# Kernel optimization log

Measured on AMD Instinct MI355X. Metric: run time of the kernel, lower is better.

## Reference

```python
import jax, jax.numpy as jnp
import numpy as np

B, F0, D = 1024, 32, 32
HID = [128, 128, 128]


def setup_inputs() -> dict:
    key = jax.random.key(0)
    ks = jax.random.split(key, 4)
    inputs = jax.random.normal(ks[0], (B, F0, D), dtype=jnp.float32)
    # glorot-like init for conv filters, flattened to (F0*Fk, H)
    def glorot(k, fan_in, fan_out):
        lim = np.sqrt(6.0 / (fan_in + fan_out)).astype(np.float32)
        return jax.random.uniform(k, (fan_in, fan_out), dtype=jnp.float32, minval=-lim, maxval=lim)
    W0 = glorot(ks[1], F0 * F0, HID[0])
    W1 = glorot(ks[2], F0 * HID[0], HID[1])
    W2 = glorot(ks[3], F0 * HID[1], HID[2])
    b0 = jnp.zeros((HID[0],), dtype=jnp.float32)
    b1 = jnp.zeros((HID[1],), dtype=jnp.float32)
    b2 = jnp.zeros((HID[2],), dtype=jnp.float32)
    return {"inputs": inputs, "W0": W0, "W1": W1, "W2": W2,
            "b0": b0, "b1": b1, "b2": b2,
            "field_size": F0, "embedding_size": D}


def _cin_layer(x0, state, W, b):
    # x0: (B, F0, D), state: (B, Fk, D)
    bsz, f0, d = x0.shape
    fk = state.shape[1]
    # per-embedding-dim outer product; flatten (f0, fk) row-major to match
    # tf reshape of matmul(state_split_0, state_split_k^T)
    z = jnp.einsum('bfd,bgd->bdfg', x0, state).reshape(bsz, d, f0 * fk)
    h = z @ W + b  # (B, D, H); 1x1 conv1d == matmul over f0*fk
    # activation is linear (identity)
    return jnp.transpose(h, (0, 2, 1))  # (B, H, D)


def reference(inputs, W0, W1, W2, b0, b1, b2, field_size, embedding_size):
    x0 = inputs.reshape(-1, field_size, embedding_size)
    state = x0
    outputs = []
    for W, b in ((W0, b0), (W1, b1), (W2, b2)):
        fm = _cin_layer(x0, state, W, b)
        state = fm          # skip=False: state and output are the full map
        outputs.append(fm)
    # concat over field axis, sum over embedding dim -> (B, sum(H))
    return jnp.sum(jnp.concatenate(outputs, axis=1), axis=-1)
```

## Files before the change

### kernel.cpp

```cpp
#include <hip/hip_runtime.h>
#include <hip/hip_bf16.h>


typedef __attribute__((ext_vector_type(8))) short short8;
typedef __attribute__((ext_vector_type(8))) __bf16 bf16x8;
typedef __attribute__((ext_vector_type(16))) float f32x16;
typedef __attribute__((ext_vector_type(4))) unsigned short u16x4;

#define DEVINL static __device__ __forceinline__

DEVINL unsigned short f2bf_rne(float f) {
  unsigned int u = __builtin_bit_cast(unsigned int, f);
  unsigned int r = u + 0x7fffu + ((u >> 16) & 1u);
  return (unsigned short)(r >> 16);
}

template <typename V>
DEVINL auto mfma_32x32x16_bf16(V a, V b, f32x16 c, int)
    -> decltype(__builtin_amdgcn_mfma_f32_32x32x16_bf16(a, b, c, 0, 0, 0)) {
  return __builtin_amdgcn_mfma_f32_32x32x16_bf16(a, b, c, 0, 0, 0);
}
template <typename V>
DEVINL f32x16 mfma_32x32x16_bf16(V a, V b, f32x16 c, long) {
  return __builtin_amdgcn_mfma_f32_32x32x16_bf16(
      __builtin_bit_cast(bf16x8, a), __builtin_bit_cast(bf16x8, b), c, 0, 0, 0);
}
DEVINL f32x16 mfma_bf16(short8 a, short8 b, f32x16 c) {
  return mfma_32x32x16_bf16(a, b, c, 0);
}

__global__ void pack_w_kernel(const float* __restrict__ W0,
                              const float* __restrict__ W1,
                              const float* __restrict__ W2,
                              unsigned short* __restrict__ Wt) {
  __shared__ float tile[8][132];
  const int u = blockIdx.x;
  const float* W; int FK, f, kb, base;
  if (u < 128)      { W = W0; FK = 32;  f = u >> 2;         kb = u & 3;          base = 0; }
  else if (u < 640) { W = W1; FK = 128; f = (u - 128) >> 4; kb = (u - 128) & 15; base = 131072; }
  else              { W = W2; FK = 128; f = (u - 640) >> 4; kb = (u - 640) & 15; base = 655360; }
  const int t = threadIdx.x;
#pragma unroll
  for (int i = 0; i < 4; ++i) {
    const int e = t + i * 256;
    const int kk = e >> 7, h = e & 127;
    tile[kk][h] = W[(f * FK + kb * 8 + kk) * 128 + h];
  }
  __syncthreads();
  unsigned short* dst = Wt + base + f * (FK / 8) * 1024 + kb * 1024;
  const int h = t >> 1;
  const int j0 = (t & 1) * 4;
  u16x4 v;
  v.x = f2bf_rne(tile[j0 + 0][h]);
  v.y = f2bf_rne(tile[j0 + 1][h]);
  v.z = f2bf_rne(tile[j0 + 2][h]);
  v.w = f2bf_rne(tile[j0 + 3][h]);
  *(u16x4*)&dst[t * 4] = v;
}

template <int KQ, int LAYER>
DEVINL void run_layer(const unsigned short* __restrict__ WtL,
                      const float* __restrict__ bias,
                      const float* __restrict__ x0g,
                      float* __restrict__ outp, int outoff,
                      unsigned int* SB,
                      int wgb0, int mrow, int bw, int l31, int half) {
  __syncthreads();

  int4 sfr[KQ];
  const int r = bw * 32 + l31;
#pragma unroll
  for (int kq = 0; kq < KQ; ++kq) {
    const int row0 = kq * 8 + half * 4;
    int4 v;
    v.x = (int)SB[(row0 + 0) * 128 + r];
    v.y = (int)SB[(row0 + 1) * 128 + r];
    v.z = (int)SB[(row0 + 2) * 128 + r];
    v.w = (int)SB[(row0 + 3) * 128 + r];
    sfr[kq] = v;
  }

  f32x16 zv;
#pragma unroll
  for (int e = 0; e < 16; ++e) zv[e] = 0.f;
  f32x16 outacc = zv;

  const char* gb = (const char*)WtL +
                   (size_t)(half * 2048 + (mrow * 32 + l31) * 16);
  const int xb = (wgb0 + bw) * 1024 + l31;

  auto ldq = [&](short8* wv, int q) {
#pragma unroll
    for (int i = 0; i < 4; ++i)
      wv[i] = *(const short8*)(gb + (size_t)q * 16384 + i * 4096);
  };

  short8 wa[4], wb[4];

  if constexpr (KQ == 8) {
    float xs = x0g[xb];
    ldq(wa, 0);
    ldq(wb, 1);
    __syncthreads();

#pragma unroll 1
    for (int f = 0; f < 32; ++f) {
      float xn = xs;
      if (f < 31) xn = x0g[xb + (f + 1) * 32];
      f32x16 Y;
#pragma unroll
      for (int i = 0; i < 4; ++i) {
        const short8 s = __builtin_bit_cast(short8, sfr[i]);
        Y = mfma_bf16(wa[i], s, i == 0 ? zv : Y);
      }
      if (f < 31) ldq(wa, 2 * f + 2);
#pragma unroll
      for (int i = 0; i < 4; ++i) {
        const short8 s = __builtin_bit_cast(short8, sfr[4 + i]);
        Y = mfma_bf16(wb[i], s, Y);
      }
      if (f < 31) ldq(wb, 2 * f + 3);
#pragma unroll
      for (int e = 0; e < 16; ++e) outacc[e] += xs * Y[e];
      xs = xn;
    }
  } else {
    float xa0 = x0g[xb], xa1 = x0g[xb + 32];
    ldq(wa, 0);
    __syncthreads();

    const short8 s0 = __builtin_bit_cast(short8, sfr[0]);
    const short8 s1 = __builtin_bit_cast(short8, sfr[KQ - 1]);
    auto doQ = [&](const short8* wv, float xA, float xB) {
      f32x16 Y = mfma_bf16(wv[0], s0, zv);
      Y = mfma_bf16(wv[1], s1, Y);
#pragma unroll
      for (int e = 0; e < 16; ++e) outacc[e] += xA * Y[e];
      Y = mfma_bf16(wv[2], s0, zv);
      Y = mfma_bf16(wv[3], s1, Y);
#pragma unroll
      for (int e = 0; e < 16; ++e) outacc[e] += xB * Y[e];
    };

#pragma unroll 1
    for (int q2 = 0; q2 < 8; ++q2) {
      const int q = 2 * q2;
      const float xm0 = x0g[xb + (2 * q + 2) * 32];
      const float xm1 = x0g[xb + (2 * q + 3) * 32];
      ldq(wb, q + 1);
      float xn0 = xa0, xn1 = xa1;
      if (q2 < 7) {
        xn0 = x0g[xb + (2 * q + 4) * 32];
        xn1 = x0g[xb + (2 * q + 5) * 32];
      }
      doQ(wa, xa0, xa1);
      if (q2 < 7) ldq(wa, q + 2);
      doQ(wb, xm0, xm1);
      xa0 = xn0; xa1 = xn1;
    }
  }

  float bv[16];
#pragma unroll
  for (int e = 0; e < 16; ++e)
    bv[e] = bias[mrow * 32 + (e & 3) + 8 * (e >> 2) + 4 * half];

  if constexpr (LAYER < 2) {
#pragma unroll
    for (int g = 0; g < 4; ++g) {
      const int h2 = mrow * 16 + 4 * g + 2 * half;
      const float v0 = outacc[4 * g + 0] + bv[4 * g + 0];
      const float v1 = outacc[4 * g + 1] + bv[4 * g + 1];
      const float v2 = outacc[4 * g + 2] + bv[4 * g + 2];
      const float v3 = outacc[4 * g + 3] + bv[4 * g + 3];
      SB[h2 * 128 + r] = (unsigned)f2bf_rne(v0) | ((unsigned)f2bf_rne(v1) << 16);
      SB[(h2 + 1) * 128 + r] =
          (unsigned)f2bf_rne(v2) | ((unsigned)f2bf_rne(v3) << 16);
    }
  }

  float sv[16];
#pragma unroll
  for (int e = 0; e < 16; ++e) {
    float v = outacc[e];
    v += __shfl_xor(v, 1);
    v += __shfl_xor(v, 2);
    v += __shfl_xor(v, 4);
    v += __shfl_xor(v, 8);
    v += __shfl_xor(v, 16);
    sv[e] = v + 32.0f * bv[e];
  }
  if (l31 == 0) {
#pragma unroll
    for (int g = 0; g < 4; ++g) {
      const int h = mrow * 32 + 8 * g + 4 * half;
      float4 o = {sv[4 * g + 0], sv[4 * g + 1], sv[4 * g + 2], sv[4 * g + 3]};
      *(float4*)&outp[bw * 384 + outoff + h] = o;
    }
  }
}

DEVINL void run_layer2_fast(const unsigned short* __restrict__ WtL,
                            const float* __restrict__ bias,
                            const float* __restrict__ x0g,
                            float* __restrict__ outp,
                            unsigned int* SB, int wgb0,
                            int w, int l31, int half, int tid) {
  __syncthreads();

  f32x16 zv;
#pragma unroll
  for (int e = 0; e < 16; ++e) zv[e] = 0.f;

  const int bw = w >> 2, gt = w & 3;
  short8 a1[2];
  {
    const float* xr = &x0g[(size_t)(wgb0 + bw) * 1024 + l31 * 32];
#pragma unroll
    for (int kq = 0; kq < 2; ++kq) {
      const int d0 = kq * 16 + half * 8;
      union { short8 v; unsigned short u[8]; } t;
#pragma unroll
      for (int j = 0; j < 8; ++j) t.u[j] = f2bf_rne(xr[d0 + j]);
      a1[kq] = t.v;
    }
  }
  short8 bfr[2];
  {
    const int g = gt * 32 + l31;
    const unsigned int* row = &SB[(g >> 1) * 128 + bw * 32];
    const int sh = (g & 1) * 16;
#pragma unroll
    for (int kq = 0; kq < 2; ++kq) {
      const int d0 = kq * 16 + half * 8;
      union { short8 v; unsigned short u[8]; } t;
#pragma unroll
      for (int j = 0; j < 8; ++j)
        t.u[j] = (unsigned short)(row[d0 + j] >> sh);
      bfr[kq] = t.v;
    }
  }
  f32x16 ua = mfma_bf16(a1[0], bfr[0], zv);
  ua = mfma_bf16(a1[1], bfr[1], ua);
  __syncthreads();

  unsigned short* U16 = (unsigned short*)SB;
  {
    const int g = gt * 32 + l31;
#pragma unroll
    for (int reg = 0; reg < 16; ++reg) {
      const int f = (reg & 3) + 8 * (reg >> 2) + 4 * half;
      const int k = f * 128 + g;
      U16[(k >> 1) * 8 + bw * 2 + (k & 1)] = f2bf_rne(ua[reg]);
    }
  }
  __syncthreads();

  const int mt = w & 3, kh = w >> 2;
  const char* gb = (const char*)WtL +
                   (size_t)(half * 2048 + (mt * 32 + l31) * 16);
  const int bl = l31 & 3;

  auto ldq2 = [&](short8* wv, int q) {
#pragma unroll
    for (int i = 0; i < 4; ++i)
      wv[i] = *(const short8*)(gb + (size_t)q * 16384 + i * 4096);
  };
  auto breadq = [&](short8* bv, int q) {
#pragma unroll
    for (int i = 0; i < 4; ++i) {
      const int row0 = (q * 4 + i) * 8 + half * 4;
      int4 v;
      v.x = (int)SB[(row0 + 0) * 4 + bl];
      v.y = (int)SB[(row0 + 1) * 4 + bl];
      v.z = (int)SB[(row0 + 2) * 4 + bl];
      v.w = (int)SB[(row0 + 3) * 4 + bl];
      bv[i] = __builtin_bit_cast(short8, v);
    }
  };

  f32x16 acc0 = zv, acc1 = zv;
  short8 qa[4], qb[4], Ba[4], Bb[4];
  const int q0 = kh * 16;
  ldq2(qa, q0);
  breadq(Ba, q0);
#pragma unroll 1
  for (int qq = 0; qq < 8; ++qq) {
    const int q = q0 + 2 * qq;
    ldq2(qb, q + 1);
    breadq(Bb, q + 1);
#pragma unroll
    for (int i = 0; i < 4; ++i) acc0 = mfma_bf16(qa[i], Ba[i], acc0);
    if (qq < 7) {
      ldq2(qa, q + 2);
      breadq(Ba, q + 2);
    }
#pragma unroll
    for (int i = 0; i < 4; ++i) acc1 = mfma_bf16(qb[i], Bb[i], acc1);
  }
#pragma unroll
  for (int e = 0; e < 16; ++e) acc0[e] += acc1[e];

  __syncthreads();

  float* P = (float*)SB;
  if (l31 < 4) {
#pragma unroll
    for (int reg = 0; reg < 16; ++reg) {
      const int h = mt * 32 + (reg & 3) + 8 * (reg >> 2) + 4 * half;
      P[(l31 * 128 + h) * 4 + kh] = acc0[reg];
    }
  }
  __syncthreads();
  if (tid < 512) {
    const int b = tid >> 7, h = tid & 127;
    const float v = P[tid * 4] + P[tid * 4 + 1] + P[tid * 4 + 2] +
                    P[tid * 4 + 3] + 32.0f * bias[h];
    outp[b * 384 + 256 + h] = v;
  }
}

__global__ __launch_bounds__(1024, 1) void cin_kernel(
    const float* __restrict__ x0g, const unsigned short* __restrict__ Wt,
    const float* __restrict__ b0, const float* __restrict__ b1,
    const float* __restrict__ b2, float* __restrict__ out) {
  __shared__ unsigned int SB[64 * 128];

  const int t = threadIdx.x;
  const int lane = t & 63;
  const int w = t >> 6;
  const int mrow = w & 3;
  const int bw = w >> 2;
  const int l31 = lane & 31, half = lane >> 5;
  const int wgb0 = blockIdx.x * 4;

#pragma unroll
  for (int s = 0; s < 2; ++s) {
    const int i = t + s * 1024;
    const int r = i & 127, g2 = i >> 7;
    const float* p = &x0g[(wgb0 + (r >> 5)) * 1024 + (2 * g2) * 32 + (r & 31)];
    SB[g2 * 128 + r] =
        (unsigned)f2bf_rne(p[0]) | ((unsigned)f2bf_rne(p[32]) << 16);
  }

  float* outp = out + (size_t)wgb0 * 384;
  run_layer<2, 0>(Wt, b0, x0g, outp, 0, SB, wgb0, mrow, bw, l31, half);
  run_layer<8, 1>(Wt + 131072, b1, x0g, outp, 128, SB,
                  wgb0, mrow, bw, l31, half);
  run_layer2_fast(Wt + 655360, b2, x0g, outp, SB, wgb0, w, l31, half, t);
}

extern "C" void kernel_launch(void* const* d_in, const int* in_sizes, int n_in,
                              void* d_out, int out_size, void* d_ws, size_t ws_size,
                              hipStream_t stream) {
  (void)in_sizes; (void)n_in; (void)out_size; (void)ws_size;
  const float* x0 = (const float*)d_in[0];
  const float* W0 = (const float*)d_in[1];
  const float* W1 = (const float*)d_in[2];
  const float* W2 = (const float*)d_in[3];
  const float* b0 = (const float*)d_in[4];
  const float* b1 = (const float*)d_in[5];
  const float* b2 = (const float*)d_in[6];
  unsigned short* Wt = (unsigned short*)d_ws;

  pack_w_kernel<<<1152, 256, 0, stream>>>(W0, W1, W2, Wt);
  cin_kernel<<<256, 1024, 0, stream>>>(x0, Wt, b0, b1, b2, (float*)d_out);
}
```

Baseline: 143.6 us.

## Split K across wave pairs, share weight fragments over two batches, stage x0 in LDS

Layers 0 and 1 now give each wave two batch rows and half of the K range. Each loaded weight fragment feeds MFMAs for both batches, which halves global weight traffic per MFMA. The two K halves are then reduced through a new shared-memory partial buffer with extra barriers. x0 for the block is copied into LDS with global_load_lds so the per-field scalar x reads come from shared memory instead of global. The change adds LDS usage (x0 plus the partial-sum buffer) and synchronization for the cross-wave reduction.

```diff
diff --git a/kernel.cpp b/kernel.cpp
--- a/kernel.cpp
+++ b/kernel.cpp
@@ -13,6 +13,12 @@
   unsigned int u = __builtin_bit_cast(unsigned int, f);
   unsigned int r = u + 0x7fffu + ((u >> 16) & 1u);
   return (unsigned short)(r >> 16);
+}
+
+DEVINL void gload_lds16(const void* g, void* l) {
+  __builtin_amdgcn_global_load_lds(
+      (const __attribute__((address_space(1))) unsigned int*)g,
+      (__attribute__((address_space(3))) unsigned int*)l, 16, 0, 0);
 }
 
 template <typename V>
@@ -58,153 +64,154 @@
   *(u16x4*)&dst[t * 4] = v;
 }
 
-template <int KQ, int LAYER>
+template <int KQH, int LAYER>
 DEVINL void run_layer(const unsigned short* __restrict__ WtL,
                       const float* __restrict__ bias,
-                      const float* __restrict__ x0g,
+                      const float* x0l,
                       float* __restrict__ outp, int outoff,
-                      unsigned int* SB,
-                      int wgb0, int mrow, int bw, int l31, int half) {
-  __syncthreads();
-
-  int4 sfr[KQ];
-  const int r = bw * 32 + l31;
-#pragma unroll
-  for (int kq = 0; kq < KQ; ++kq) {
-    const int row0 = kq * 8 + half * 4;
-    int4 v;
-    v.x = (int)SB[(row0 + 0) * 128 + r];
-    v.y = (int)SB[(row0 + 1) * 128 + r];
-    v.z = (int)SB[(row0 + 2) * 128 + r];
-    v.w = (int)SB[(row0 + 3) * 128 + r];
-    sfr[kq] = v;
+                      unsigned int* SB, float* PS,
+                      int mrow, int npair, int kh, int l31, int half) {
+  __syncthreads();
+
+  int4 sfr[2][KQH];
+  const int rb = npair * 64;
+#pragma unroll
+  for (int nt = 0; nt < 2; ++nt) {
+    const int r = rb + nt * 32 + l31;
+#pragma unroll
+    for (int i = 0; i < KQH; ++i) {
+      const int row0 = (kh * KQH + i) * 8 + half * 4;
+      int4 v;
+      v.x = (int)SB[(row0 + 0) * 128 + r];
+      v.y = (int)SB[(row0 + 1) * 128 + r];
+      v.z = (int)SB[(row0 + 2) * 128 + r];
+      v.w = (int)SB[(row0 + 3) * 128 + r];
+      sfr[nt][i] = v;
+    }
   }
 
   f32x16 zv;
 #pragma unroll
   for (int e = 0; e < 16; ++e) zv[e] = 0.f;
-  f32x16 outacc = zv;
-
-  const char* gb = (const char*)WtL +
-                   (size_t)(half * 2048 + (mrow * 32 + l31) * 16);
-  const int xb = (wgb0 + bw) * 1024 + l31;
-
-  auto ldq = [&](short8* wv, int q) {
-#pragma unroll
-    for (int i = 0; i < 4; ++i)
-      wv[i] = *(const short8*)(gb + (size_t)q * 16384 + i * 4096);
-  };
-
-  short8 wa[4], wb[4];
-
-  if constexpr (KQ == 8) {
-    float xs = x0g[xb];
-    ldq(wa, 0);
-    ldq(wb, 1);
+  f32x16 acc[2] = {zv, zv};
+
+  constexpr int FSTRIDE = KQH * 8192;
+  const char* gp = (const char*)WtL +
+                   (size_t)(kh * KQH * 4096 + half * 2048 +
+                            (mrow * 32 + l31) * 16);
+  const int xb0 = (npair * 2) * 1024 + l31;
+  const int xb1 = xb0 + 1024;
+
+  short8 qa[KQH];
+#pragma unroll
+  for (int i = 0; i < KQH; ++i)
+    qa[i] = *(const short8*)(gp + i * 4096);
+  float xs0 = x0l[xb0], xs1 = x0l[xb1];
+  __syncthreads();
+
+#pragma unroll 1
+  for (int f = 0; f < 32; ++f) {
+    f32x16 Y;
+#pragma unroll
+    for (int i = 0; i < KQH; ++i) {
+      const short8 s = __builtin_bit_cast(short8, sfr[0][i]);
+      Y = mfma_bf16(qa[i], s, i == 0 ? zv : Y);
+    }
+#pragma unroll
+    for (int e = 0; e < 16; ++e) acc[0][e] += xs0 * Y[e];
+#pragma unroll
+    for (int i = 0; i < KQH; ++i) {
+      const short8 s = __builtin_bit_cast(short8, sfr[1][i]);
+      Y = mfma_bf16(qa[i], s, i == 0 ? zv : Y);
+    }
+    if (f < 31) {
+      gp += FSTRIDE;
+#pragma unroll
+      for (int i = 0; i < KQH; ++i)
+        qa[i] = *(const short8*)(gp + i * 4096);
+    }
+#pragma unroll
+    for (int e = 0; e < 16; ++e) acc[1][e] += xs1 * Y[e];
+    if (f < 31) {
+      xs0 = x0l[xb0 + (f + 1) * 32];
+      xs1 = x0l[xb1 + (f + 1) * 32];
+    }
+  }
+
+  const int psb = (mrow * 2 + npair) * 1024 + half * 512 + l31;
+#pragma unroll 1
+  for (int nt = 0; nt < 2; ++nt) {
+    if (kh == 1) {
+#pragma unroll
+      for (int reg = 0; reg < 16; ++reg)
+        PS[psb + reg * 32] = acc[nt][reg];
+    }
     __syncthreads();
-
-#pragma unroll 1
-    for (int f = 0; f < 32; ++f) {
-      float xn = xs;
-      if (f < 31) xn = x0g[xb + (f + 1) * 32];
-      f32x16 Y;
-#pragma unroll
-      for (int i = 0; i < 4; ++i) {
-        const short8 s = __builtin_bit_cast(short8, sfr[i]);
-        Y = mfma_bf16(wa[i], s, i == 0 ? zv : Y);
+    if (kh == 0) {
+#pragma unroll
+      for (int reg = 0; reg < 16; ++reg)
+        acc[nt][reg] += PS[psb + reg * 32];
+    }
+    __syncthreads();
+  }
+
+  if (kh == 0) {
+    float bv[16];
+#pragma unroll
+    for (int e = 0; e < 16; ++e)
+      bv[e] = bias[mrow * 32 + (e & 3) + 8 * (e >> 2) + 4 * half];
+
+    if constexpr (LAYER < 2) {
+#pragma unroll
+      for (int nt = 0; nt < 2; ++nt) {
+        const int r = rb + nt * 32 + l31;
+#pragma unroll
+        for (int g = 0; g < 4; ++g) {
+          const int h2 = mrow * 16 + 4 * g + 2 * half;
+          const float v0 = acc[nt][4 * g + 0] + bv[4 * g + 0];
+          const float v1 = acc[nt][4 * g + 1] + bv[4 * g + 1];
+          const float v2 = acc[nt][4 * g + 2] + bv[4 * g + 2];
+          const float v3 = acc[nt][4 * g + 3] + bv[4 * g + 3];
+          SB[h2 * 128 + r] =
+              (unsigned)f2bf_rne(v0) | ((unsigned)f2bf_rne(v1) << 16);
+          SB[(h2 + 1) * 128 + r] =
+              (unsigned)f2bf_rne(v2) | ((unsigned)f2bf_rne(v3) << 16);
+        }
       }
-      if (f < 31) ldq(wa, 2 * f + 2);
-#pragma unroll
-      for (int i = 0; i < 4; ++i) {
-        const short8 s = __builtin_bit_cast(short8, sfr[4 + i]);
-        Y = mfma_bf16(wb[i], s, Y);
+    }
+
+#pragma unroll
+    for (int nt = 0; nt < 2; ++nt) {
+      float sv[16];
+#pragma unroll
+      for (int e = 0; e < 16; ++e) {
+        float v = acc[nt][e];
+        v += __shfl_xor(v, 1);
+        v += __shfl_xor(v, 2);
+        v += __shfl_xor(v, 4);
+        v += __shfl_xor(v, 8);
+        v += __shfl_xor(v, 16);
+        sv[e] = v + 32.0f * bv[e];
       }
-      if (f < 31) ldq(wb, 2 * f + 3);
-#pragma unroll
-      for (int e = 0; e < 16; ++e) outacc[e] += xs * Y[e];
-      xs = xn;
-    }
-  } else {
-    float xa0 = x0g[xb], xa1 = x0g[xb + 32];
-    ldq(wa, 0);
-    __syncthreads();
-
-    const short8 s0 = __builtin_bit_cast(short8, sfr[0]);
-    const short8 s1 = __builtin_bit_cast(short8, sfr[KQ - 1]);
-    auto doQ = [&](const short8* wv, float xA, float xB) {
-      f32x16 Y = mfma_bf16(wv[0], s0, zv);
-      Y = mfma_bf16(wv[1], s1, Y);
-#pragma unroll
-      for (int e = 0; e < 16; ++e) outacc[e] += xA * Y[e];
-      Y = mfma_bf16(wv[2], s0, zv);
-      Y = mfma_bf16(wv[3], s1, Y);
-#pragma unroll
-      for (int e = 0; e < 16; ++e) outacc[e] += xB * Y[e];
-    };
-
-#pragma unroll 1
-    for (int q2 = 0; q2 < 8; ++q2) {
-      const int q = 2 * q2;
-      const float xm0 = x0g[xb + (2 * q + 2) * 32];
-      const float xm1 = x0g[xb + (2 * q + 3) * 32];
-      ldq(wb, q + 1);
-      float xn0 = xa0, xn1 = xa1;
-      if (q2 < 7) {
-        xn0 = x0g[xb + (2 * q + 4) * 32];
-        xn1 = x0g[xb + (2 * q + 5) * 32];
+      if (l31 == 0) {
+        const int b = npair * 2 + nt;
+#pragma unroll
+        for (int g = 0; g < 4; ++g) {
+          const int h = mrow * 32 + 8 * g + 4 * half;
+          float4 o = {sv[4 * g + 0], sv[4 * g + 1], sv[4 * g + 2],
+                      sv[4 * g + 3]};
+          *(float4*)&outp[b * 384 + outoff + h] = o;
+        }
       }
-      doQ(wa, xa0, xa1);
-      if (q2 < 7) ldq(wa, q + 2);
-      doQ(wb, xm0, xm1);
-      xa0 = xn0; xa1 = xn1;
-    }
-  }
-
-  float bv[16];
-#pragma unroll
-  for (int e = 0; e < 16; ++e)
-    bv[e] = bias[mrow * 32 + (e & 3) + 8 * (e >> 2) + 4 * half];
-
-  if constexpr (LAYER < 2) {
-#pragma unroll
-    for (int g = 0; g < 4; ++g) {
-      const int h2 = mrow * 16 + 4 * g + 2 * half;
-      const float v0 = outacc[4 * g + 0] + bv[4 * g + 0];
-      const float v1 = outacc[4 * g + 1] + bv[4 * g + 1];
-      const float v2 = outacc[4 * g + 2] + bv[4 * g + 2];
-      const float v3 = outacc[4 * g + 3] + bv[4 * g + 3];
-      SB[h2 * 128 + r] = (unsigned)f2bf_rne(v0) | ((unsigned)f2bf_rne(v1) << 16);
-      SB[(h2 + 1) * 128 + r] =
-          (unsigned)f2bf_rne(v2) | ((unsigned)f2bf_rne(v3) << 16);
-    }
-  }
-
-  float sv[16];
-#pragma unroll
-  for (int e = 0; e < 16; ++e) {
-    float v = outacc[e];
-    v += __shfl_xor(v, 1);
-    v += __shfl_xor(v, 2);
-    v += __shfl_xor(v, 4);
-    v += __shfl_xor(v, 8);
-    v += __shfl_xor(v, 16);
-    sv[e] = v + 32.0f * bv[e];
-  }
-  if (l31 == 0) {
-#pragma unroll
-    for (int g = 0; g < 4; ++g) {
-      const int h = mrow * 32 + 8 * g + 4 * half;
-      float4 o = {sv[4 * g + 0], sv[4 * g + 1], sv[4 * g + 2], sv[4 * g + 3]};
-      *(float4*)&outp[bw * 384 + outoff + h] = o;
     }
   }
 }
 
 DEVINL void run_layer2_fast(const unsigned short* __restrict__ WtL,
                             const float* __restrict__ bias,
-                            const float* __restrict__ x0g,
+                            const float* x0l,
                             float* __restrict__ outp,
-                            unsigned int* SB, int wgb0,
+                            unsigned int* SB, float* PS,
                             int w, int l31, int half, int tid) {
   __syncthreads();
 
@@ -215,7 +222,7 @@
   const int bw = w >> 2, gt = w & 3;
   short8 a1[2];
   {
-    const float* xr = &x0g[(size_t)(wgb0 + bw) * 1024 + l31 * 32];
+    const float* xr = &x0l[bw * 1024 + l31 * 32];
 #pragma unroll
     for (int kq = 0; kq < 2; ++kq) {
       const int d0 = kq * 16 + half * 8;
@@ -256,7 +263,7 @@
   }
   __syncthreads();
 
-  const int mt = w & 3, kh = w >> 2;
+  const int mt = w & 3, kh4 = w >> 2;
   const char* gb = (const char*)WtL +
                    (size_t)(half * 2048 + (mt * 32 + l31) * 16);
   const int bl = l31 & 3;
@@ -281,7 +288,7 @@
 
   f32x16 acc0 = zv, acc1 = zv;
   short8 qa[4], qb[4], Ba[4], Bb[4];
-  const int q0 = kh * 16;
+  const int q0 = kh4 * 16;
   ldq2(qa, q0);
   breadq(Ba, q0);
 #pragma unroll 1
@@ -303,12 +310,12 @@
 
   __syncthreads();
 
-  float* P = (float*)SB;
+  float* P = PS;
   if (l31 < 4) {
 #pragma unroll
     for (int reg = 0; reg < 16; ++reg) {
       const int h = mt * 32 + (reg & 3) + 8 * (reg >> 2) + 4 * half;
-      P[(l31 * 128 + h) * 4 + kh] = acc0[reg];
+      P[(l31 * 128 + h) * 4 + kh4] = acc0[reg];
     }
   }
   __syncthreads();
@@ -325,15 +332,20 @@
     const float* __restrict__ b0, const float* __restrict__ b1,
     const float* __restrict__ b2, float* __restrict__ out) {
   __shared__ unsigned int SB[64 * 128];
+  __shared__ __align__(16) float x0l[4096];
+  __shared__ float PS[8192];
 
   const int t = threadIdx.x;
   const int lane = t & 63;
   const int w = t >> 6;
   const int mrow = w & 3;
-  const int bw = w >> 2;
+  const int kh = (w >> 2) & 1;
+  const int npair = w >> 3;
   const int l31 = lane & 31, half = lane >> 5;
   const int wgb0 = blockIdx.x * 4;
 
+  const float* xsrc = x0g + (size_t)wgb0 * 1024;
+  gload_lds16(xsrc + w * 256 + lane * 4, x0l + w * 256);
 #pragma unroll
   for (int s = 0; s < 2; ++s) {
     const int i = t + s * 1024;
@@ -344,10 +356,10 @@
   }
 
   float* outp = out + (size_t)wgb0 * 384;
-  run_layer<2, 0>(Wt, b0, x0g, outp, 0, SB, wgb0, mrow, bw, l31, half);
-  run_layer<8, 1>(Wt + 131072, b1, x0g, outp, 128, SB,
-                  wgb0, mrow, bw, l31, half);
-  run_layer2_fast(Wt + 655360, b2, x0g, outp, SB, wgb0, w, l31, half, t);
+  run_layer<1, 0>(Wt, b0, x0l, outp, 0, SB, PS, mrow, npair, kh, l31, half);
+  run_layer<4, 1>(Wt + 131072, b1, x0l, outp, 128, SB, PS,
+                  mrow, npair, kh, l31, half);
+  run_layer2_fast(Wt + 655360, b2, x0l, outp, SB, PS, w, l31, half, t);
 }
 
 extern "C" void kernel_launch(void* const* d_in, const int* in_sizes, int n_in,
```

Result: no change. 145.3 us (+1.1%).
